# Kernel tuning notes

Hardware: AMD Instinct MI355X
Metric: run time of the kernel (lower is better)

The kernel has to match this reference:

```python
import jax, jax.numpy as jnp
import numpy as np

N = 50000        # nodes
E_RAND = 800000  # random edges (avg degree 16)
F_IN = 512       # num_features
H = 128          # h_dim * num_heads = 16 * 8
C = 40           # num_classes
NEG_SLOPE = 0.2  # GATv2 default


def _glorot(key, shape):
    lim = float(np.sqrt(6.0 / (shape[0] + shape[1])))
    return jax.random.uniform(key, shape, jnp.float32, -lim, lim)


def setup_inputs() -> dict:
    key = jax.random.key(0)
    ks = jax.random.split(key, 12)
    src = jax.random.randint(ks[0], (E_RAND,), 0, N)
    dst = jax.random.randint(ks[1], (E_RAND,), 0, N)
    loop = jnp.arange(N)  # self-loops (GATv2Conv add_self_loops=True)
    edge_index = jnp.stack([jnp.concatenate([src, loop]),
                            jnp.concatenate([dst, loop])]).astype(jnp.int32)
    x = jax.random.normal(ks[2], (N, F_IN), jnp.float32)
    return {
        "x": x,
        "edge_index": edge_index,
        "W1l": _glorot(ks[3], (F_IN, H)), "b1l": jnp.zeros((H,), jnp.float32),
        "W1r": _glorot(ks[4], (F_IN, H)), "b1r": jnp.zeros((H,), jnp.float32),
        "a1": _glorot(ks[5], (H, 1)).reshape(H),
        "bias1": jnp.zeros((H,), jnp.float32),
        "W2l": _glorot(ks[6], (H, C)), "b2l": jnp.zeros((C,), jnp.float32),
        "W2r": _glorot(ks[7], (H, C)), "b2r": jnp.zeros((C,), jnp.float32),
        "a2": _glorot(ks[8], (C, 1)).reshape(C),
        "bias2": jnp.zeros((C,), jnp.float32),
    }


def gatv2_layer(x, src, dst, Wl, bl, Wr, br, att, bias, n):
    # PyG GATv2Conv, heads=1: xl = lin_l(x) (source side), xr = lin_r(x) (target side)
    xl = x @ Wl + bl                                   # [N, C_out]
    xr = x @ Wr + br                                   # [N, C_out]
    # edge score e_ij = a^T LeakyReLU(xl[j] + xr[i])
    e = jax.nn.leaky_relu(xl[src] + xr[dst], negative_slope=NEG_SLOPE) @ att  # [E]
    # segment softmax over edges grouped by destination node
    m = jax.ops.segment_max(e, dst, num_segments=n)    # every node has a self-loop
    ex = jnp.exp(e - m[dst])
    den = jax.ops.segment_sum(ex, dst, num_segments=n)
    alpha = ex / den[dst]                              # [E]
    # weighted scatter-aggregate of source-transformed features
    out = jax.ops.segment_sum(alpha[:, None] * xl[src], dst, num_segments=n)
    return out + bias


def reference(x, edge_index, W1l, b1l, W1r, b1r, a1, bias1,
              W2l, b2l, W2r, b2r, a2, bias2):
    # eval mode: dropout(p=0.6) is identity
    src, dst = edge_index[0], edge_index[1]
    n = x.shape[0]
    h = gatv2_layer(x, src, dst, W1l, b1l, W1r, b1r, a1, bias1, n)
    h = jax.nn.elu(h)
    h = gatv2_layer(h, src, dst, W2l, b2l, W2r, b2r, a2, bias2, n)
    return (h, jax.nn.log_softmax(h, axis=1))
```

## Files before the change

### kernel.cpp

```cpp
#include <hip/hip_runtime.h>
#include <hip/hip_bf16.h>
#include <math.h>

#define FIN 512
#define H1 128
#define C2 40
#define C2P 64

typedef __attribute__((ext_vector_type(8))) short short8;
typedef __attribute__((ext_vector_type(4))) float f32x4;

__device__ __forceinline__ ushort f2bf(float f) {
    union { float f; unsigned u; } c; c.f = f;
    unsigned u = c.u;
    return (ushort)((u + 0x7fffu + ((u >> 16) & 1u)) >> 16);
}
__device__ __forceinline__ float bf2f_lo(unsigned u) { return __uint_as_float(u << 16); }
__device__ __forceinline__ float bf2f_hi(unsigned u) { return __uint_as_float(u & 0xffff0000u); }

__device__ __forceinline__ short bfc(float f) {
    __hip_bfloat16 h = __float2bfloat16(f);
    return *reinterpret_cast<short*>(&h);
}

__device__ __forceinline__ void gload_lds16(const void* g, void* l) {
    __builtin_amdgcn_global_load_lds(
        (const __attribute__((address_space(1))) void*)g,
        (__attribute__((address_space(3))) void*)l, 16, 0, 0);
}

__global__ void count_k(const int* __restrict__ dst, int* __restrict__ cnt, int E) {
    int e = blockIdx.x * 256 + threadIdx.x;
    if (e < E) atomicAdd(&cnt[dst[e] + 1], 1);
}

__global__ __launch_bounds__(1024) void scan_k(int* __restrict__ arr, int ntot) {
    __shared__ int part[1024];
    int t = threadIdx.x;
    int chunk = (((ntot + 1023) / 1024) + 3) & ~3;
    int b = t * chunk;
    int s = 0;
    bool full = (b + chunk <= ntot);
    if (full) {
#pragma unroll 4
        for (int j = 0; j < chunk; j += 4) {
            int4 v = *reinterpret_cast<const int4*>(&arr[b + j]);
            s += v.x + v.y + v.z + v.w;
        }
    } else {
        for (int j = b; j < ntot; j++) s += arr[j];
    }
    part[t] = s;
    __syncthreads();
    for (int off = 1; off < 1024; off <<= 1) {
        int v = (t >= off) ? part[t - off] : 0;
        __syncthreads();
        part[t] += v;
        __syncthreads();
    }
    int run = (t == 0) ? 0 : part[t - 1];
    if (full) {
        for (int j = 0; j < chunk; j += 4) {
            int4 v = *reinterpret_cast<const int4*>(&arr[b + j]);
            int r0 = run + v.x, r1 = r0 + v.y, r2 = r1 + v.z, r3 = r2 + v.w;
            *reinterpret_cast<int4*>(&arr[b + j]) = make_int4(r0, r1, r2, r3);
            run = r3;
        }
    } else {
        for (int j = b; j < ntot; j++) { run += arr[j]; arr[j] = run; }
    }
}

__global__ void fill_k(const int* __restrict__ src, const int* __restrict__ dst,
                       const int* __restrict__ rowptr, int* __restrict__ fillp,
                       int* __restrict__ csr, int E) {
    int e = blockIdx.x * 256 + threadIdx.x;
    if (e < E) {
        int d = dst[e];
        int p = atomicAdd(&fillp[d], 1);
        csr[rowptr[d] + p] = src[e];
    }
}

__global__ void prep_k(const float* __restrict__ W1l, const float* __restrict__ W1r,
                       ushort* __restrict__ Wt2) {
    int idx = blockIdx.x * 256 + threadIdx.x;
    int kc  = idx >> 11;
    int rem = idx & 2047;
    int col = rem >> 3;
    int j   = rem & 7;
    int k   = kc * 8 + j;
    float v = (col < H1) ? W1l[k * H1 + col] : W1r[k * H1 + (col - H1)];
    Wt2[idx] = f2bf(v);
}

__global__ void prep2_k(const float* __restrict__ W2l, const float* __restrict__ W2r,
                        ushort* __restrict__ Ws) {
    int idx = blockIdx.x * 256 + threadIdx.x;
    if (idx >= 80 * H1) return;
    int col = idx >> 7;
    int k   = idx & 127;
    float v = (col < C2) ? W2l[k * C2 + col] : W2r[k * C2 + (col - C2)];
    Ws[idx] = f2bf(v);
}

__global__ __launch_bounds__(256, 3) void gemm1_k(
    const float* __restrict__ x, const ushort* __restrict__ Wt2,
    const float* __restrict__ bl, const float* __restrict__ br,
    ushort* __restrict__ xlb, float* __restrict__ xr, int n)
{
    __shared__ ushort As[64][72];
    __shared__ ushort Bs[8 * 256 * 8];

    const int tid  = threadIdx.x;
    const int w    = tid >> 6;
    const int lane = tid & 63;
    const int l15  = lane & 15;
    const int lhi  = lane >> 4;
    const int r0   = blockIdx.x * 64;

    f32x4 acc[4][4];
#pragma unroll
    for (int m = 0; m < 4; m++)
#pragma unroll
        for (int nn = 0; nn < 4; nn++) acc[m][nn] = (f32x4){0.f, 0.f, 0.f, 0.f};

    const int arow = tid >> 2;
    const int akq  = (tid & 3) * 16;
    const int arow_g = min(r0 + arow, n - 1);
    const float* aptr = x + (size_t)arow_g * FIN + akq;

    const char* bsrc = (const char*)Wt2 + (size_t)w * 8192 + (size_t)lane * 16;
    char*       bdst = (char*)Bs + (size_t)w * 8192 + (size_t)lane * 16;

    for (int kk = 0; kk < FIN; kk += 64) {
        const char* bs = bsrc + (size_t)(kk >> 3) * 4096;
#pragma unroll
        for (int i = 0; i < 8; i++)
            gload_lds16(bs + i * 1024, bdst + i * 1024);

        float4 v0 = *reinterpret_cast<const float4*>(aptr + kk);
        float4 v1 = *reinterpret_cast<const float4*>(aptr + kk + 4);
        float4 v2 = *reinterpret_cast<const float4*>(aptr + kk + 8);
        float4 v3 = *reinterpret_cast<const float4*>(aptr + kk + 12);
        short8 h0, h1;
        h0[0] = bfc(v0.x); h0[1] = bfc(v0.y); h0[2] = bfc(v0.z); h0[3] = bfc(v0.w);
        h0[4] = bfc(v1.x); h0[5] = bfc(v1.y); h0[6] = bfc(v1.z); h0[7] = bfc(v1.w);
        h1[0] = bfc(v2.x); h1[1] = bfc(v2.y); h1[2] = bfc(v2.z); h1[3] = bfc(v2.w);
        h1[4] = bfc(v3.x); h1[5] = bfc(v3.y); h1[6] = bfc(v3.z); h1[7] = bfc(v3.w);
        *reinterpret_cast<short8*>(&As[arow][akq])     = h0;
        *reinterpret_cast<short8*>(&As[arow][akq + 8]) = h1;

        __syncthreads();

#pragma unroll
        for (int ks = 0; ks < 2; ks++) {
            short8 af[4], bf4[4];
#pragma unroll
            for (int m = 0; m < 4; m++)
                af[m] = *reinterpret_cast<const short8*>(&As[m * 16 + l15][ks * 32 + lhi * 8]);
#pragma unroll
            for (int nn = 0; nn < 4; nn++)
                bf4[nn] = *reinterpret_cast<const short8*>(
                    &Bs[((ks * 4 + lhi) * 256 + w * 64 + nn * 16 + l15) * 8]);
#pragma unroll
            for (int m = 0; m < 4; m++)
#pragma unroll
                for (int nn = 0; nn < 4; nn++)
                    acc[m][nn] = __builtin_amdgcn_mfma_f32_16x16x32_bf16(af[m], bf4[nn], acc[m][nn], 0, 0, 0);
        }
        __syncthreads();
    }

#pragma unroll
    for (int nn = 0; nn < 4; nn++) {
        int col = w * 64 + nn * 16 + l15;
        bool left = (col < H1);
        float bias = left ? bl[col] : br[col - H1];
#pragma unroll
        for (int m = 0; m < 4; m++) {
#pragma unroll
            for (int r = 0; r < 4; r++) {
                int row = r0 + m * 16 + lhi * 4 + r;
                if (row < n) {
                    float v = acc[m][nn][r] + bias;
                    if (left) xlb[(size_t)row * H1 + col] = f2bf(v);
                    else      xr [(size_t)row * H1 + (col - H1)] = v;
                }
            }
        }
    }
}

__global__ __launch_bounds__(256) void edge1_k(
    const ushort* __restrict__ xlb, const float* xr,
    const int* __restrict__ rowptr, const int* __restrict__ csr,
    const float* __restrict__ att, const float* __restrict__ bias,
    float* h, int n)
{
    int wid  = threadIdx.x >> 6;
    int lane = threadIdx.x & 63;
    int grp  = lane >> 4;
    int gl   = lane & 15;
    int i = blockIdx.x * 4 + wid;
    if (i >= n) return;

    const float* xrp = &xr[(size_t)i * H1 + gl * 8];
    float4 xr0 = *reinterpret_cast<const float4*>(xrp);
    float4 xr1v = *reinterpret_cast<const float4*>(xrp + 4);
    float xrv[8] = {xr0.x, xr0.y, xr0.z, xr0.w, xr1v.x, xr1v.y, xr1v.z, xr1v.w};
    float4 a0 = *reinterpret_cast<const float4*>(&att[gl * 8]);
    float4 a1 = *reinterpret_cast<const float4*>(&att[gl * 8 + 4]);
    float av[8] = {a0.x, a0.y, a0.z, a0.w, a1.x, a1.y, a1.z, a1.w};

    int e0 = rowptr[i], e1 = rowptr[i + 1];

    float m = -INFINITY, den = 0.f;
    float acc[8];
#pragma unroll
    for (int f = 0; f < 8; f++) acc[f] = 0.f;

    int e = e0 + grp;
    uint4 u;
    if (e < e1) {
        int s = csr[e];
        u = *reinterpret_cast<const uint4*>(&xlb[(size_t)s * H1 + gl * 8]);
    }
    while (e < e1) {
        uint4 cu = u;
        int en = e + 4;
        if (en < e1) {
            int s2 = csr[en];
            u = *reinterpret_cast<const uint4*>(&xlb[(size_t)s2 * H1 + gl * 8]);
        }
        float xlv[8];
        xlv[0] = bf2f_lo(cu.x); xlv[1] = bf2f_hi(cu.x);
        xlv[2] = bf2f_lo(cu.y); xlv[3] = bf2f_hi(cu.y);
        xlv[4] = bf2f_lo(cu.z); xlv[5] = bf2f_hi(cu.z);
        xlv[6] = bf2f_lo(cu.w); xlv[7] = bf2f_hi(cu.w);
        float p = 0.f;
#pragma unroll
        for (int f = 0; f < 8; f++) {
            float t = xlv[f] + xrv[f];
            t = t > 0.f ? t : 0.2f * t;
            p += t * av[f];
        }
#pragma unroll
        for (int o = 8; o > 0; o >>= 1) p += __shfl_xor(p, o);
        float mn = fmaxf(m, p);
        float sc = __expf(m - mn);
        float wgt = __expf(p - mn);
        den = den * sc + wgt;
#pragma unroll
        for (int f = 0; f < 8; f++) acc[f] = acc[f] * sc + wgt * xlv[f];
        m = mn;
        e = en;
    }

    float mstar = m;
    mstar = fmaxf(mstar, __shfl_xor(mstar, 16));
    mstar = fmaxf(mstar, __shfl_xor(mstar, 32));
    float scale = __expf(m - mstar);
    den *= scale;
#pragma unroll
    for (int f = 0; f < 8; f++) acc[f] *= scale;
    den += __shfl_xor(den, 16); den += __shfl_xor(den, 32);
#pragma unroll
    for (int f = 0; f < 8; f++) {
        acc[f] += __shfl_xor(acc[f], 16);
        acc[f] += __shfl_xor(acc[f], 32);
    }

    if (grp == 0) {
        float inv = 1.f / den;
        float o[8];
#pragma unroll
        for (int f = 0; f < 8; f++) {
            float v = acc[f] * inv + bias[gl * 8 + f];
            o[f] = v > 0.f ? v : expm1f(v);
        }
        float* hp = &h[(size_t)i * H1 + gl * 8];
        *reinterpret_cast<float4*>(hp)     = make_float4(o[0], o[1], o[2], o[3]);
        *reinterpret_cast<float4*>(hp + 4) = make_float4(o[4], o[5], o[6], o[7]);
    }
}

__global__ __launch_bounds__(256) void gemm2_k(
    const float* __restrict__ h, const ushort* __restrict__ Ws,
    const float* __restrict__ bl, const float* __restrict__ br,
    ushort* __restrict__ xl2b, float* __restrict__ xr2, int n)
{
    __shared__ ushort WsL[80][136];

    const int tid = threadIdx.x;
    const int w    = tid >> 6;
    const int lane = tid & 63;
    const int l15  = lane & 15;
    const int lhi  = lane >> 4;
    const int r0 = blockIdx.x * 64;

#pragma unroll
    for (int q = 0; q < 5; q++) {
        int c = tid + q * 256;
        int col = c >> 4;
        int k0  = (c & 15) * 8;
        *reinterpret_cast<short8*>(&WsL[col][k0]) =
            *reinterpret_cast<const short8*>(&Ws[col * H1 + k0]);
    }
    __syncthreads();

    const int arow = min(r0 + w * 16 + l15, n - 1);
    const float* ap = &h[(size_t)arow * H1 + lhi * 8];

    f32x4 acc[5];
#pragma unroll
    for (int nt = 0; nt < 5; nt++) acc[nt] = (f32x4){0.f, 0.f, 0.f, 0.f};

#pragma unroll
    for (int kc = 0; kc < 4; kc++) {
        float4 v0 = *reinterpret_cast<const float4*>(ap + kc * 32);
        float4 v1 = *reinterpret_cast<const float4*>(ap + kc * 32 + 4);
        short8 af;
        af[0] = bfc(v0.x); af[1] = bfc(v0.y);
        af[2] = bfc(v0.z); af[3] = bfc(v0.w);
        af[4] = bfc(v1.x); af[5] = bfc(v1.y);
        af[6] = bfc(v1.z); af[7] = bfc(v1.w);
#pragma unroll
        for (int nt = 0; nt < 5; nt++) {
            short8 bf = *reinterpret_cast<const short8*>(&WsL[nt * 16 + l15][kc * 32 + lhi * 8]);
            acc[nt] = __builtin_amdgcn_mfma_f32_16x16x32_bf16(af, bf, acc[nt], 0, 0, 0);
        }
    }

#pragma unroll
    for (int nt = 0; nt < 5; nt++) {
        int col = nt * 16 + l15;
        float bias = (col < C2) ? bl[col] : br[col - C2];
#pragma unroll
        for (int r = 0; r < 4; r++) {
            int row = r0 + w * 16 + lhi * 4 + r;
            if (row < n) {
                float v = acc[nt][r] + bias;
                if (col < C2) xl2b[(size_t)row * C2P + col] = f2bf(v);
                else          xr2 [(size_t)row * C2  + (col - C2)] = v;
            }
        }
    }
    {
        int row = r0 + w * 16 + l15;
        int part = lhi;
        if (part < 3 && row < n) {
            uint4 z = make_uint4(0u, 0u, 0u, 0u);
            *reinterpret_cast<uint4*>(&xl2b[(size_t)row * C2P + C2 + part * 8]) = z;
        }
    }
}

__global__ __launch_bounds__(256) void edge2_k(
    const ushort* __restrict__ xl2b, const float* __restrict__ xr2,
    const int* __restrict__ rowptr, const int* __restrict__ csr,
    const float* __restrict__ att, const float* __restrict__ bias,
    float* __restrict__ out, int n)
{
    int wid  = threadIdx.x >> 6;
    int lane = threadIdx.x & 63;
    int grp  = lane >> 3;
    int gl   = lane & 7;
    int i = blockIdx.x * 4 + wid;
    if (i >= n) return;

    float xrv[8], av[8];
#pragma unroll
    for (int f = 0; f < 8; f++) {
        int idx = gl * 8 + f;
        bool real = idx < C2;
        xrv[f] = real ? xr2[(size_t)i * C2 + idx] : 0.f;
        av[f]  = real ? att[idx] : 0.f;
    }

    int e0 = rowptr[i], e1 = rowptr[i + 1];

    float m = -INFINITY, den = 0.f;
    float acc[8];
#pragma unroll
    for (int f = 0; f < 8; f++) acc[f] = 0.f;

    int e = e0 + grp;
    uint4 u;
    if (e < e1) {
        int s = csr[e];
        u = *reinterpret_cast<const uint4*>(&xl2b[(size_t)s * C2P + gl * 8]);
    }
    while (e < e1) {
        uint4 cu = u;
        int en = e + 8;
        if (en < e1) {
            int s2 = csr[en];
            u = *reinterpret_cast<const uint4*>(&xl2b[(size_t)s2 * C2P + gl * 8]);
        }
        float xlv[8];
        xlv[0] = bf2f_lo(cu.x); xlv[1] = bf2f_hi(cu.x);
        xlv[2] = bf2f_lo(cu.y); xlv[3] = bf2f_hi(cu.y);
        xlv[4] = bf2f_lo(cu.z); xlv[5] = bf2f_hi(cu.z);
        xlv[6] = bf2f_lo(cu.w); xlv[7] = bf2f_hi(cu.w);
        float p = 0.f;
#pragma unroll
        for (int f = 0; f < 8; f++) {
            float t = xlv[f] + xrv[f];
            t = t > 0.f ? t : 0.2f * t;
            p += t * av[f];
        }
#pragma unroll
        for (int o = 4; o > 0; o >>= 1) p += __shfl_xor(p, o);
        float mn = fmaxf(m, p);
        float sc = __expf(m - mn);
        float wgt = __expf(p - mn);
        den = den * sc + wgt;
#pragma unroll
        for (int f = 0; f < 8; f++) acc[f] = acc[f] * sc + wgt * xlv[f];
        m = mn;
        e = en;
    }

    float mstar = m;
    mstar = fmaxf(mstar, __shfl_xor(mstar, 8));
    mstar = fmaxf(mstar, __shfl_xor(mstar, 16));
    mstar = fmaxf(mstar, __shfl_xor(mstar, 32));
    float scale = __expf(m - mstar);
    den *= scale;
#pragma unroll
    for (int f = 0; f < 8; f++) acc[f] *= scale;
    den += __shfl_xor(den, 8); den += __shfl_xor(den, 16); den += __shfl_xor(den, 32);
#pragma unroll
    for (int f = 0; f < 8; f++) {
        acc[f] += __shfl_xor(acc[f], 8);
        acc[f] += __shfl_xor(acc[f], 16);
        acc[f] += __shfl_xor(acc[f], 32);
    }

    float inv = 1.f / den;
    bool real_lane = gl < 5;
    float o[8];
#pragma unroll
    for (int f = 0; f < 8; f++) {
        int idx = gl * 8 + f;
        o[f] = acc[f] * inv + (idx < C2 ? bias[idx] : 0.f);
    }

    float mv = -INFINITY;
    if (real_lane) {
#pragma unroll
        for (int f = 0; f < 8; f++) mv = fmaxf(mv, o[f]);
    }
    mv = fmaxf(mv, __shfl_xor(mv, 1));
    mv = fmaxf(mv, __shfl_xor(mv, 2));
    mv = fmaxf(mv, __shfl_xor(mv, 4));
    float se = 0.f;
    if (real_lane) {
#pragma unroll
        for (int f = 0; f < 8; f++) se += __expf(o[f] - mv);
    }
    se += __shfl_xor(se, 1); se += __shfl_xor(se, 2); se += __shfl_xor(se, 4);
    float lse = mv + logf(se);

    if (grp == 0 && real_lane) {
        float* op = &out[(size_t)i * C2 + gl * 8];
        *reinterpret_cast<float4*>(op)     = make_float4(o[0], o[1], o[2], o[3]);
        *reinterpret_cast<float4*>(op + 4) = make_float4(o[4], o[5], o[6], o[7]);
        float* lp = &out[(size_t)n * C2 + (size_t)i * C2 + gl * 8];
        *reinterpret_cast<float4*>(lp)     = make_float4(o[0] - lse, o[1] - lse, o[2] - lse, o[3] - lse);
        *reinterpret_cast<float4*>(lp + 4) = make_float4(o[4] - lse, o[5] - lse, o[6] - lse, o[7] - lse);
    }
}

extern "C" void kernel_launch(void* const* d_in, const int* in_sizes, int n_in,
                              void* d_out, int out_size, void* d_ws, size_t ws_size,
                              hipStream_t stream) {
    const float* x    = (const float*)d_in[0];
    const int*   ei   = (const int*)  d_in[1];
    const float* W1l  = (const float*)d_in[2];
    const float* b1l  = (const float*)d_in[3];
    const float* W1r  = (const float*)d_in[4];
    const float* b1r  = (const float*)d_in[5];
    const float* a1   = (const float*)d_in[6];
    const float* bias1= (const float*)d_in[7];
    const float* W2l  = (const float*)d_in[8];
    const float* b2l  = (const float*)d_in[9];
    const float* W2r  = (const float*)d_in[10];
    const float* b2r  = (const float*)d_in[11];
    const float* a2   = (const float*)d_in[12];
    const float* bias2= (const float*)d_in[13];

    const int N = in_sizes[0] / FIN;
    const int E = in_sizes[1] / 2;
    const int* src = ei;
    const int* dst = ei + E;

    float*  xr1 = (float*)d_ws;
    float*  xr2 = xr1 + (size_t)N * H1;
    ushort* xlb = (ushort*)(xr2 + (size_t)N * C2);
    ushort* xl2b = xlb;
    ushort* Wt2 = xlb + (size_t)N * H1;
    ushort* Ws2 = Wt2 + 131072;
    int* rowptr = (int*)(Ws2 + 10240);
    int* fillp  = rowptr + (N + 1);
    int* csr    = fillp + N;

    hipMemsetAsync(rowptr, 0, sizeof(int) * (size_t)(2 * N + 1), stream);
    count_k<<<(E + 255) / 256, 256, 0, stream>>>(dst, rowptr, E);
    scan_k<<<1, 1024, 0, stream>>>(rowptr, N + 1);
    fill_k<<<(E + 255) / 256, 256, 0, stream>>>(src, dst, rowptr, fillp, csr, E);

    prep_k<<<512, 256, 0, stream>>>(W1l, W1r, Wt2);
    prep2_k<<<40, 256, 0, stream>>>(W2l, W2r, Ws2);
    gemm1_k<<<(N + 63) / 64, 256, 0, stream>>>(x, Wt2, b1l, b1r, xlb, xr1, N);
    edge1_k<<<(N + 3) / 4, 256, 0, stream>>>(xlb, xr1, rowptr, csr, a1, bias1, xr1, N);
    gemm2_k<<<(N + 63) / 64, 256, 0, stream>>>(xr1, Ws2, b2l, b2r, xl2b, xr2, N);
    edge2_k<<<(N + 3) / 4, 256, 0, stream>>>(xl2b, xr2, rowptr, csr, a2, bias2, (float*)d_out, N);
}
```

Baseline: 294.6 us.

## Double-buffer GEMM1 LDS tiles and deepen gather prefetch in aggregation kernels

The first-layer GEMM moves from single-buffered 64-wide K tiles to double-buffered 32-wide K tiles. The next tile's global-to-LDS loads and x conversion are issued before the MFMAs on the current tile, and one barrier per step replaces two. Both edge-aggregation kernels now prefetch the gathered source features two iterations ahead instead of one, to hide more gather latency. The cost is more register pressure from the extra uint4 buffer, and the GEMM runs twice as many, smaller iterations.

```diff
diff --git a/kernel.cpp b/kernel.cpp
--- a/kernel.cpp
+++ b/kernel.cpp
@@ -109,8 +109,8 @@
     const float* __restrict__ bl, const float* __restrict__ br,
     ushort* __restrict__ xlb, float* __restrict__ xr, int n)
 {
-    __shared__ ushort As[64][72];
-    __shared__ ushort Bs[8 * 256 * 8];
+    __shared__ ushort As[2][64][40];
+    __shared__ ushort Bs[2][4 * 256 * 8];
 
     const int tid  = threadIdx.x;
     const int w    = tid >> 6;
@@ -126,50 +126,77 @@
         for (int nn = 0; nn < 4; nn++) acc[m][nn] = (f32x4){0.f, 0.f, 0.f, 0.f};
 
     const int arow = tid >> 2;
-    const int akq  = (tid & 3) * 16;
+    const int akq  = (tid & 3) * 8;
     const int arow_g = min(r0 + arow, n - 1);
     const float* aptr = x + (size_t)arow_g * FIN + akq;
 
-    const char* bsrc = (const char*)Wt2 + (size_t)w * 8192 + (size_t)lane * 16;
-    char*       bdst = (char*)Bs + (size_t)w * 8192 + (size_t)lane * 16;
-
-    for (int kk = 0; kk < FIN; kk += 64) {
-        const char* bs = bsrc + (size_t)(kk >> 3) * 4096;
-#pragma unroll
-        for (int i = 0; i < 8; i++)
-            gload_lds16(bs + i * 1024, bdst + i * 1024);
-
-        float4 v0 = *reinterpret_cast<const float4*>(aptr + kk);
-        float4 v1 = *reinterpret_cast<const float4*>(aptr + kk + 4);
-        float4 v2 = *reinterpret_cast<const float4*>(aptr + kk + 8);
-        float4 v3 = *reinterpret_cast<const float4*>(aptr + kk + 12);
-        short8 h0, h1;
+    const char* bsrc = (const char*)Wt2 + (size_t)tid * 16;
+    char*       bdst = (char*)Bs + (size_t)tid * 16;
+
+    {
+        float4 v0 = *reinterpret_cast<const float4*>(aptr);
+        float4 v1 = *reinterpret_cast<const float4*>(aptr + 4);
+#pragma unroll
+        for (int i = 0; i < 4; i++)
+            gload_lds16(bsrc + i * 4096, bdst + i * 4096);
+        short8 h0;
         h0[0] = bfc(v0.x); h0[1] = bfc(v0.y); h0[2] = bfc(v0.z); h0[3] = bfc(v0.w);
         h0[4] = bfc(v1.x); h0[5] = bfc(v1.y); h0[6] = bfc(v1.z); h0[7] = bfc(v1.w);
-        h1[0] = bfc(v2.x); h1[1] = bfc(v2.y); h1[2] = bfc(v2.z); h1[3] = bfc(v2.w);
-        h1[4] = bfc(v3.x); h1[5] = bfc(v3.y); h1[6] = bfc(v3.z); h1[7] = bfc(v3.w);
-        *reinterpret_cast<short8*>(&As[arow][akq])     = h0;
-        *reinterpret_cast<short8*>(&As[arow][akq + 8]) = h1;
+        *reinterpret_cast<short8*>(&As[0][arow][akq]) = h0;
+    }
+    __syncthreads();
+
+    int cur = 0;
+    for (int t = 0; t < 15; ++t) {
+        const int nxt = cur ^ 1;
+
+        float4 v0 = *reinterpret_cast<const float4*>(aptr + (t + 1) * 32);
+        float4 v1 = *reinterpret_cast<const float4*>(aptr + (t + 1) * 32 + 4);
+        {
+            const char* bs = bsrc + (size_t)(t + 1) * 16384;
+            char*       bd = bdst + (size_t)nxt * 16384;
+#pragma unroll
+            for (int i = 0; i < 4; i++)
+                gload_lds16(bs + i * 4096, bd + i * 4096);
+        }
+
+        short8 af[4], bf4[4];
+#pragma unroll
+        for (int m = 0; m < 4; m++)
+            af[m] = *reinterpret_cast<const short8*>(&As[cur][m * 16 + l15][lhi * 8]);
+#pragma unroll
+        for (int nn = 0; nn < 4; nn++)
+            bf4[nn] = *reinterpret_cast<const short8*>(
+                &Bs[cur][(lhi * 256 + w * 64 + nn * 16 + l15) * 8]);
+#pragma unroll
+        for (int m = 0; m < 4; m++)
+#pragma unroll
+            for (int nn = 0; nn < 4; nn++)
+                acc[m][nn] = __builtin_amdgcn_mfma_f32_16x16x32_bf16(af[m], bf4[nn], acc[m][nn], 0, 0, 0);
+
+        short8 h0;
+        h0[0] = bfc(v0.x); h0[1] = bfc(v0.y); h0[2] = bfc(v0.z); h0[3] = bfc(v0.w);
+        h0[4] = bfc(v1.x); h0[5] = bfc(v1.y); h0[6] = bfc(v1.z); h0[7] = bfc(v1.w);
+        *reinterpret_cast<short8*>(&As[nxt][arow][akq]) = h0;
 
         __syncthreads();
-
-#pragma unroll
-        for (int ks = 0; ks < 2; ks++) {
-            short8 af[4], bf4[4];
-#pragma unroll
-            for (int m = 0; m < 4; m++)
-                af[m] = *reinterpret_cast<const short8*>(&As[m * 16 + l15][ks * 32 + lhi * 8]);
+        cur = nxt;
+    }
+
+    {
+        short8 af[4], bf4[4];
+#pragma unroll
+        for (int m = 0; m < 4; m++)
+            af[m] = *reinterpret_cast<const short8*>(&As[cur][m * 16 + l15][lhi * 8]);
+#pragma unroll
+        for (int nn = 0; nn < 4; nn++)
+            bf4[nn] = *reinterpret_cast<const short8*>(
+                &Bs[cur][(lhi * 256 + w * 64 + nn * 16 + l15) * 8]);
+#pragma unroll
+        for (int m = 0; m < 4; m++)
 #pragma unroll
             for (int nn = 0; nn < 4; nn++)
-                bf4[nn] = *reinterpret_cast<const short8*>(
-                    &Bs[((ks * 4 + lhi) * 256 + w * 64 + nn * 16 + l15) * 8]);
-#pragma unroll
-            for (int m = 0; m < 4; m++)
-#pragma unroll
-                for (int nn = 0; nn < 4; nn++)
-                    acc[m][nn] = __builtin_amdgcn_mfma_f32_16x16x32_bf16(af[m], bf4[nn], acc[m][nn], 0, 0, 0);
-        }
-        __syncthreads();
+                acc[m][nn] = __builtin_amdgcn_mfma_f32_16x16x32_bf16(af[m], bf4[nn], acc[m][nn], 0, 0, 0);
     }
 
 #pragma unroll
@@ -221,17 +248,21 @@
     for (int f = 0; f < 8; f++) acc[f] = 0.f;
 
     int e = e0 + grp;
-    uint4 u;
+    uint4 u0, u1;
     if (e < e1) {
         int s = csr[e];
-        u = *reinterpret_cast<const uint4*>(&xlb[(size_t)s * H1 + gl * 8]);
+        u0 = *reinterpret_cast<const uint4*>(&xlb[(size_t)s * H1 + gl * 8]);
+    }
+    if (e + 4 < e1) {
+        int s = csr[e + 4];
+        u1 = *reinterpret_cast<const uint4*>(&xlb[(size_t)s * H1 + gl * 8]);
     }
     while (e < e1) {
-        uint4 cu = u;
-        int en = e + 4;
-        if (en < e1) {
-            int s2 = csr[en];
-            u = *reinterpret_cast<const uint4*>(&xlb[(size_t)s2 * H1 + gl * 8]);
+        uint4 cu = u0;
+        u0 = u1;
+        if (e + 8 < e1) {
+            int s2 = csr[e + 8];
+            u1 = *reinterpret_cast<const uint4*>(&xlb[(size_t)s2 * H1 + gl * 8]);
         }
         float xlv[8];
         xlv[0] = bf2f_lo(cu.x); xlv[1] = bf2f_hi(cu.x);
@@ -254,7 +285,7 @@
 #pragma unroll
         for (int f = 0; f < 8; f++) acc[f] = acc[f] * sc + wgt * xlv[f];
         m = mn;
-        e = en;
+        e += 4;
     }
 
     float mstar = m;
@@ -386,17 +417,21 @@
     for (int f = 0; f < 8; f++) acc[f] = 0.f;
 
     int e = e0 + grp;
-    uint4 u;
+    uint4 u0, u1;
     if (e < e1) {
         int s = csr[e];
-        u = *reinterpret_cast<const uint4*>(&xl2b[(size_t)s * C2P + gl * 8]);
+        u0 = *reinterpret_cast<const uint4*>(&xl2b[(size_t)s * C2P + gl * 8]);
+    }
+    if (e + 8 < e1) {
+        int s = csr[e + 8];
+        u1 = *reinterpret_cast<const uint4*>(&xl2b[(size_t)s * C2P + gl * 8]);
     }
     while (e < e1) {
-        uint4 cu = u;
-        int en = e + 8;
-        if (en < e1) {
-            int s2 = csr[en];
-            u = *reinterpret_cast<const uint4*>(&xl2b[(size_t)s2 * C2P + gl * 8]);
+        uint4 cu = u0;
+        u0 = u1;
+        if (e + 16 < e1) {
+            int s2 = csr[e + 16];
+            u1 = *reinterpret_cast<const uint4*>(&xl2b[(size_t)s2 * C2P + gl * 8]);
         }
         float xlv[8];
         xlv[0] = bf2f_lo(cu.x); xlv[1] = bf2f_hi(cu.x);
@@ -419,7 +454,7 @@
 #pragma unroll
         for (int f = 0; f < 8; f++) acc[f] = acc[f] * sc + wgt * xlv[f];
         m = mn;
-        e = en;
+        e += 8;
     }
 
     float mstar = m;
```

Result: slower. 306.3 us (+4.0%).

## Fuse layer-2 linear into edge1 aggregation and merge prep kernels into count

Applied to the files above, without the earlier changes.

Merges the count, weight-prep and layer-2 weight-prep kernels into one launch, and fuses the second GEMM into the first edge kernel. Each wave now computes its node's h row, stages it in LDS and does the 128x80 dot products with scalar FMAs, so the fp32 h tensor is never written to or read back from global memory. Edge1 switches to 8 lanes per edge with 16 features each and a two-deep gather prefetch, and edge2 gets the same deeper prefetch. The cost is more register pressure, per-block weight loading into LDS in edge1, and scalar FMAs in place of MFMA for the small GEMM. xl2b gets its own workspace buffer instead of aliasing xlb.

```diff
diff --git a/kernel.cpp b/kernel.cpp
--- a/kernel.cpp
+++ b/kernel.cpp
@@ -17,6 +17,9 @@
 }
 __device__ __forceinline__ float bf2f_lo(unsigned u) { return __uint_as_float(u << 16); }
 __device__ __forceinline__ float bf2f_hi(unsigned u) { return __uint_as_float(u & 0xffff0000u); }
+__device__ __forceinline__ float bf2f_s(short s) {
+    return __uint_as_float(((unsigned)(ushort)s) << 16);
+}
 
 __device__ __forceinline__ short bfc(float f) {
     __hip_bfloat16 h = __float2bfloat16(f);
@@ -29,9 +32,34 @@
         (__attribute__((address_space(3))) void*)l, 16, 0, 0);
 }
 
-__global__ void count_k(const int* __restrict__ dst, int* __restrict__ cnt, int E) {
-    int e = blockIdx.x * 256 + threadIdx.x;
-    if (e < E) atomicAdd(&cnt[dst[e] + 1], 1);
+__global__ void aux_k(const int* __restrict__ dst, int* __restrict__ cnt, int E, int EB,
+                      const float* __restrict__ W1l, const float* __restrict__ W1r,
+                      ushort* __restrict__ Wt2,
+                      const float* __restrict__ W2l, const float* __restrict__ W2r,
+                      ushort* __restrict__ Ws) {
+    int b = blockIdx.x;
+    int t = threadIdx.x;
+    if (b < EB) {
+        int e = b * 256 + t;
+        if (e < E) atomicAdd(&cnt[dst[e] + 1], 1);
+    } else if (b < EB + 512) {
+        int idx = (b - EB) * 256 + t;
+        int kc  = idx >> 11;
+        int rem = idx & 2047;
+        int col = rem >> 3;
+        int j   = rem & 7;
+        int k   = kc * 8 + j;
+        float v = (col < H1) ? W1l[k * H1 + col] : W1r[k * H1 + (col - H1)];
+        Wt2[idx] = f2bf(v);
+    } else {
+        int idx = (b - EB - 512) * 256 + t;
+        if (idx < 80 * H1) {
+            int col = idx >> 7;
+            int k   = idx & 127;
+            float v = (col < C2) ? W2l[k * C2 + col] : W2r[k * C2 + (col - C2)];
+            Ws[idx] = f2bf(v);
+        }
+    }
 }
 
 __global__ __launch_bounds__(1024) void scan_k(int* __restrict__ arr, int ntot) {
@@ -82,28 +110,6 @@
     }
 }
 
-__global__ void prep_k(const float* __restrict__ W1l, const float* __restrict__ W1r,
-                       ushort* __restrict__ Wt2) {
-    int idx = blockIdx.x * 256 + threadIdx.x;
-    int kc  = idx >> 11;
-    int rem = idx & 2047;
-    int col = rem >> 3;
-    int j   = rem & 7;
-    int k   = kc * 8 + j;
-    float v = (col < H1) ? W1l[k * H1 + col] : W1r[k * H1 + (col - H1)];
-    Wt2[idx] = f2bf(v);
-}
-
-__global__ void prep2_k(const float* __restrict__ W2l, const float* __restrict__ W2r,
-                        ushort* __restrict__ Ws) {
-    int idx = blockIdx.x * 256 + threadIdx.x;
-    if (idx >= 80 * H1) return;
-    int col = idx >> 7;
-    int k   = idx & 127;
-    float v = (col < C2) ? W2l[k * C2 + col] : W2r[k * C2 + (col - C2)];
-    Ws[idx] = f2bf(v);
-}
-
 __global__ __launch_bounds__(256, 3) void gemm1_k(
     const float* __restrict__ x, const ushort* __restrict__ Wt2,
     const float* __restrict__ bl, const float* __restrict__ br,
@@ -193,112 +199,17 @@
 }
 
 __global__ __launch_bounds__(256) void edge1_k(
-    const ushort* __restrict__ xlb, const float* xr,
+    const ushort* __restrict__ xlb, const float* __restrict__ xr,
     const int* __restrict__ rowptr, const int* __restrict__ csr,
     const float* __restrict__ att, const float* __restrict__ bias,
-    float* h, int n)
-{
-    int wid  = threadIdx.x >> 6;
-    int lane = threadIdx.x & 63;
-    int grp  = lane >> 4;
-    int gl   = lane & 15;
-    int i = blockIdx.x * 4 + wid;
-    if (i >= n) return;
-
-    const float* xrp = &xr[(size_t)i * H1 + gl * 8];
-    float4 xr0 = *reinterpret_cast<const float4*>(xrp);
-    float4 xr1v = *reinterpret_cast<const float4*>(xrp + 4);
-    float xrv[8] = {xr0.x, xr0.y, xr0.z, xr0.w, xr1v.x, xr1v.y, xr1v.z, xr1v.w};
-    float4 a0 = *reinterpret_cast<const float4*>(&att[gl * 8]);
-    float4 a1 = *reinterpret_cast<const float4*>(&att[gl * 8 + 4]);
-    float av[8] = {a0.x, a0.y, a0.z, a0.w, a1.x, a1.y, a1.z, a1.w};
-
-    int e0 = rowptr[i], e1 = rowptr[i + 1];
-
-    float m = -INFINITY, den = 0.f;
-    float acc[8];
-#pragma unroll
-    for (int f = 0; f < 8; f++) acc[f] = 0.f;
-
-    int e = e0 + grp;
-    uint4 u;
-    if (e < e1) {
-        int s = csr[e];
-        u = *reinterpret_cast<const uint4*>(&xlb[(size_t)s * H1 + gl * 8]);
-    }
-    while (e < e1) {
-        uint4 cu = u;
-        int en = e + 4;
-        if (en < e1) {
-            int s2 = csr[en];
-            u = *reinterpret_cast<const uint4*>(&xlb[(size_t)s2 * H1 + gl * 8]);
-        }
-        float xlv[8];
-        xlv[0] = bf2f_lo(cu.x); xlv[1] = bf2f_hi(cu.x);
-        xlv[2] = bf2f_lo(cu.y); xlv[3] = bf2f_hi(cu.y);
-        xlv[4] = bf2f_lo(cu.z); xlv[5] = bf2f_hi(cu.z);
-        xlv[6] = bf2f_lo(cu.w); xlv[7] = bf2f_hi(cu.w);
-        float p = 0.f;
-#pragma unroll
-        for (int f = 0; f < 8; f++) {
-            float t = xlv[f] + xrv[f];
-            t = t > 0.f ? t : 0.2f * t;
-            p += t * av[f];
-        }
-#pragma unroll
-        for (int o = 8; o > 0; o >>= 1) p += __shfl_xor(p, o);
-        float mn = fmaxf(m, p);
-        float sc = __expf(m - mn);
-        float wgt = __expf(p - mn);
-        den = den * sc + wgt;
-#pragma unroll
-        for (int f = 0; f < 8; f++) acc[f] = acc[f] * sc + wgt * xlv[f];
-        m = mn;
-        e = en;
-    }
-
-    float mstar = m;
-    mstar = fmaxf(mstar, __shfl_xor(mstar, 16));
-    mstar = fmaxf(mstar, __shfl_xor(mstar, 32));
-    float scale = __expf(m - mstar);
-    den *= scale;
-#pragma unroll
-    for (int f = 0; f < 8; f++) acc[f] *= scale;
-    den += __shfl_xor(den, 16); den += __shfl_xor(den, 32);
-#pragma unroll
-    for (int f = 0; f < 8; f++) {
-        acc[f] += __shfl_xor(acc[f], 16);
-        acc[f] += __shfl_xor(acc[f], 32);
-    }
-
-    if (grp == 0) {
-        float inv = 1.f / den;
-        float o[8];
-#pragma unroll
-        for (int f = 0; f < 8; f++) {
-            float v = acc[f] * inv + bias[gl * 8 + f];
-            o[f] = v > 0.f ? v : expm1f(v);
-        }
-        float* hp = &h[(size_t)i * H1 + gl * 8];
-        *reinterpret_cast<float4*>(hp)     = make_float4(o[0], o[1], o[2], o[3]);
-        *reinterpret_cast<float4*>(hp + 4) = make_float4(o[4], o[5], o[6], o[7]);
-    }
-}
-
-__global__ __launch_bounds__(256) void gemm2_k(
-    const float* __restrict__ h, const ushort* __restrict__ Ws,
-    const float* __restrict__ bl, const float* __restrict__ br,
+    const ushort* __restrict__ Ws, const float* __restrict__ b2l,
+    const float* __restrict__ b2r,
     ushort* __restrict__ xl2b, float* __restrict__ xr2, int n)
 {
     __shared__ ushort WsL[80][136];
+    __shared__ float  hlds[4][128];
 
     const int tid = threadIdx.x;
-    const int w    = tid >> 6;
-    const int lane = tid & 63;
-    const int l15  = lane & 15;
-    const int lhi  = lane >> 4;
-    const int r0 = blockIdx.x * 64;
-
 #pragma unroll
     for (int q = 0; q < 5; q++) {
         int c = tid + q * 256;
@@ -309,50 +220,136 @@
     }
     __syncthreads();
 
-    const int arow = min(r0 + w * 16 + l15, n - 1);
-    const float* ap = &h[(size_t)arow * H1 + lhi * 8];
-
-    f32x4 acc[5];
-#pragma unroll
-    for (int nt = 0; nt < 5; nt++) acc[nt] = (f32x4){0.f, 0.f, 0.f, 0.f};
-
-#pragma unroll
-    for (int kc = 0; kc < 4; kc++) {
-        float4 v0 = *reinterpret_cast<const float4*>(ap + kc * 32);
-        float4 v1 = *reinterpret_cast<const float4*>(ap + kc * 32 + 4);
-        short8 af;
-        af[0] = bfc(v0.x); af[1] = bfc(v0.y);
-        af[2] = bfc(v0.z); af[3] = bfc(v0.w);
-        af[4] = bfc(v1.x); af[5] = bfc(v1.y);
-        af[6] = bfc(v1.z); af[7] = bfc(v1.w);
-#pragma unroll
-        for (int nt = 0; nt < 5; nt++) {
-            short8 bf = *reinterpret_cast<const short8*>(&WsL[nt * 16 + l15][kc * 32 + lhi * 8]);
-            acc[nt] = __builtin_amdgcn_mfma_f32_16x16x32_bf16(af, bf, acc[nt], 0, 0, 0);
-        }
-    }
-
-#pragma unroll
-    for (int nt = 0; nt < 5; nt++) {
-        int col = nt * 16 + l15;
-        float bias = (col < C2) ? bl[col] : br[col - C2];
-#pragma unroll
-        for (int r = 0; r < 4; r++) {
-            int row = r0 + w * 16 + lhi * 4 + r;
-            if (row < n) {
-                float v = acc[nt][r] + bias;
-                if (col < C2) xl2b[(size_t)row * C2P + col] = f2bf(v);
-                else          xr2 [(size_t)row * C2  + (col - C2)] = v;
+    const int wid  = tid >> 6;
+    const int lane = tid & 63;
+    const int grp  = lane >> 3;
+    const int gl   = lane & 7;
+    const int i = blockIdx.x * 4 + wid;
+    if (i >= n) return;
+
+    float xrv[16], av[16];
+    {
+        const float* p  = &xr[(size_t)i * H1 + gl * 16];
+        const float* pa = &att[gl * 16];
+#pragma unroll
+        for (int q = 0; q < 4; q++) {
+            float4 v = *reinterpret_cast<const float4*>(p + q * 4);
+            xrv[q*4+0]=v.x; xrv[q*4+1]=v.y; xrv[q*4+2]=v.z; xrv[q*4+3]=v.w;
+            float4 a = *reinterpret_cast<const float4*>(pa + q * 4);
+            av[q*4+0]=a.x; av[q*4+1]=a.y; av[q*4+2]=a.z; av[q*4+3]=a.w;
+        }
+    }
+
+    int e0 = rowptr[i], e1 = rowptr[i + 1];
+
+    float m = -INFINITY, den = 0.f;
+    float acc[16];
+#pragma unroll
+    for (int f = 0; f < 16; f++) acc[f] = 0.f;
+
+    int e = e0 + grp;
+    uint4 ua0, ub0, ua1, ub1;
+    if (e < e1) {
+        const ushort* p = &xlb[(size_t)csr[e] * H1 + gl * 16];
+        ua0 = *reinterpret_cast<const uint4*>(p);
+        ub0 = *reinterpret_cast<const uint4*>(p + 8);
+    }
+    if (e + 8 < e1) {
+        const ushort* p = &xlb[(size_t)csr[e + 8] * H1 + gl * 16];
+        ua1 = *reinterpret_cast<const uint4*>(p);
+        ub1 = *reinterpret_cast<const uint4*>(p + 8);
+    }
+    while (e < e1) {
+        uint4 ca = ua0, cb = ub0;
+        ua0 = ua1; ub0 = ub1;
+        if (e + 16 < e1) {
+            const ushort* p = &xlb[(size_t)csr[e + 16] * H1 + gl * 16];
+            ua1 = *reinterpret_cast<const uint4*>(p);
+            ub1 = *reinterpret_cast<const uint4*>(p + 8);
+        }
+        float xlv[16];
+        xlv[0]  = bf2f_lo(ca.x); xlv[1]  = bf2f_hi(ca.x);
+        xlv[2]  = bf2f_lo(ca.y); xlv[3]  = bf2f_hi(ca.y);
+        xlv[4]  = bf2f_lo(ca.z); xlv[5]  = bf2f_hi(ca.z);
+        xlv[6]  = bf2f_lo(ca.w); xlv[7]  = bf2f_hi(ca.w);
+        xlv[8]  = bf2f_lo(cb.x); xlv[9]  = bf2f_hi(cb.x);
+        xlv[10] = bf2f_lo(cb.y); xlv[11] = bf2f_hi(cb.y);
+        xlv[12] = bf2f_lo(cb.z); xlv[13] = bf2f_hi(cb.z);
+        xlv[14] = bf2f_lo(cb.w); xlv[15] = bf2f_hi(cb.w);
+        float p = 0.f;
+#pragma unroll
+        for (int f = 0; f < 16; f++) {
+            float t = xlv[f] + xrv[f];
+            t = t > 0.f ? t : 0.2f * t;
+            p += t * av[f];
+        }
+        p += __shfl_xor(p, 4); p += __shfl_xor(p, 2); p += __shfl_xor(p, 1);
+        float mn = fmaxf(m, p);
+        float sc = __expf(m - mn);
+        float wgt = __expf(p - mn);
+        den = den * sc + wgt;
+#pragma unroll
+        for (int f = 0; f < 16; f++) acc[f] = acc[f] * sc + wgt * xlv[f];
+        m = mn;
+        e += 8;
+    }
+
+    float mstar = m;
+    mstar = fmaxf(mstar, __shfl_xor(mstar, 8));
+    mstar = fmaxf(mstar, __shfl_xor(mstar, 16));
+    mstar = fmaxf(mstar, __shfl_xor(mstar, 32));
+    float scale = __expf(m - mstar);
+    den *= scale;
+#pragma unroll
+    for (int f = 0; f < 16; f++) acc[f] *= scale;
+    den += __shfl_xor(den, 8); den += __shfl_xor(den, 16); den += __shfl_xor(den, 32);
+#pragma unroll
+    for (int f = 0; f < 16; f++) {
+        acc[f] += __shfl_xor(acc[f], 8);
+        acc[f] += __shfl_xor(acc[f], 16);
+        acc[f] += __shfl_xor(acc[f], 32);
+    }
+
+    float inv = 1.f / den;
+    float o[16];
+#pragma unroll
+    for (int f = 0; f < 16; f++) {
+        float v = acc[f] * inv + bias[gl * 16 + f];
+        o[f] = v > 0.f ? v : expm1f(v);
+    }
+
+    if (grp == 0) {
+#pragma unroll
+        for (int q = 0; q < 4; q++)
+            *reinterpret_cast<float4*>(&hlds[wid][gl * 16 + q * 4]) =
+                make_float4(o[q*4], o[q*4+1], o[q*4+2], o[q*4+3]);
+    }
+
+#pragma unroll
+    for (int pass = 0; pass < 2; pass++) {
+        int c = (pass == 0) ? lane : 64 + lane;
+        bool active = (pass == 0) || (lane < 16);
+        if (active) {
+            float s2 = 0.f;
+#pragma unroll
+            for (int kb = 0; kb < 16; kb++) {
+                float4 hA = *reinterpret_cast<const float4*>(&hlds[wid][kb * 8]);
+                float4 hB = *reinterpret_cast<const float4*>(&hlds[wid][kb * 8 + 4]);
+                short8 wv = *reinterpret_cast<const short8*>(&WsL[c][kb * 8]);
+                s2 = fmaf(hA.x, bf2f_s(wv[0]), s2);
+                s2 = fmaf(hA.y, bf2f_s(wv[1]), s2);
+                s2 = fmaf(hA.z, bf2f_s(wv[2]), s2);
+                s2 = fmaf(hA.w, bf2f_s(wv[3]), s2);
+                s2 = fmaf(hB.x, bf2f_s(wv[4]), s2);
+                s2 = fmaf(hB.y, bf2f_s(wv[5]), s2);
+                s2 = fmaf(hB.z, bf2f_s(wv[6]), s2);
+                s2 = fmaf(hB.w, bf2f_s(wv[7]), s2);
             }
-        }
-    }
-    {
-        int row = r0 + w * 16 + l15;
-        int part = lhi;
-        if (part < 3 && row < n) {
-            uint4 z = make_uint4(0u, 0u, 0u, 0u);
-            *reinterpret_cast<uint4*>(&xl2b[(size_t)row * C2P + C2 + part * 8]) = z;
-        }
+            if (c < C2) xl2b[(size_t)i * C2P + c] = f2bf(s2 + b2l[c]);
+            else        xr2 [(size_t)i * C2 + (c - C2)] = s2 + b2r[c - C2];
+        }
+        if (pass == 0 && lane >= C2)
+            xl2b[(size_t)i * C2P + lane] = 0;
     }
 }
 
@@ -386,17 +383,21 @@
     for (int f = 0; f < 8; f++) acc[f] = 0.f;
 
     int e = e0 + grp;
-    uint4 u;
+    uint4 u0, u1;
     if (e < e1) {
         int s = csr[e];
-        u = *reinterpret_cast<const uint4*>(&xl2b[(size_t)s * C2P + gl * 8]);
+        u0 = *reinterpret_cast<const uint4*>(&xl2b[(size_t)s * C2P + gl * 8]);
+    }
+    if (e + 8 < e1) {
+        int s = csr[e + 8];
+        u1 = *reinterpret_cast<const uint4*>(&xl2b[(size_t)s * C2P + gl * 8]);
     }
     while (e < e1) {
-        uint4 cu = u;
-        int en = e + 8;
-        if (en < e1) {
-            int s2 = csr[en];
-            u = *reinterpret_cast<const uint4*>(&xl2b[(size_t)s2 * C2P + gl * 8]);
+        uint4 cu = u0;
+        u0 = u1;
+        if (e + 16 < e1) {
+            int s2 = csr[e + 16];
+            u1 = *reinterpret_cast<const uint4*>(&xl2b[(size_t)s2 * C2P + gl * 8]);
         }
         float xlv[8];
         xlv[0] = bf2f_lo(cu.x); xlv[1] = bf2f_hi(cu.x);
@@ -419,7 +420,7 @@
 #pragma unroll
         for (int f = 0; f < 8; f++) acc[f] = acc[f] * sc + wgt * xlv[f];
         m = mn;
-        e = en;
+        e += 8;
     }
 
     float mstar = m;
@@ -496,25 +497,25 @@
     const int* src = ei;
     const int* dst = ei + E;
 
-    float*  xr1 = (float*)d_ws;
-    float*  xr2 = xr1 + (size_t)N * H1;
-    ushort* xlb = (ushort*)(xr2 + (size_t)N * C2);
-    ushort* xl2b = xlb;
-    ushort* Wt2 = xlb + (size_t)N * H1;
-    ushort* Ws2 = Wt2 + 131072;
-    int* rowptr = (int*)(Ws2 + 10240);
-    int* fillp  = rowptr + (N + 1);
-    int* csr    = fillp + N;
+    float*  xr1  = (float*)d_ws;
+    float*  xr2  = xr1 + (size_t)N * H1;
+    ushort* xlb  = (ushort*)(xr2 + (size_t)N * C2);
+    ushort* xl2b = xlb + (size_t)N * H1;
+    ushort* Wt2  = xl2b + (size_t)N * C2P;
+    ushort* Ws2  = Wt2 + 131072;
+    int* rowptr  = (int*)(Ws2 + 10240);
+    int* fillp   = rowptr + (N + 1);
+    int* csr     = fillp + N;
+
+    const int EB = (E + 255) / 256;
 
     hipMemsetAsync(rowptr, 0, sizeof(int) * (size_t)(2 * N + 1), stream);
-    count_k<<<(E + 255) / 256, 256, 0, stream>>>(dst, rowptr, E);
+    aux_k<<<EB + 552, 256, 0, stream>>>(dst, rowptr, E, EB, W1l, W1r, Wt2, W2l, W2r, Ws2);
     scan_k<<<1, 1024, 0, stream>>>(rowptr, N + 1);
-    fill_k<<<(E + 255) / 256, 256, 0, stream>>>(src, dst, rowptr, fillp, csr, E);
-
-    prep_k<<<512, 256, 0, stream>>>(W1l, W1r, Wt2);
-    prep2_k<<<40, 256, 0, stream>>>(W2l, W2r, Ws2);
+    fill_k<<<EB, 256, 0, stream>>>(src, dst, rowptr, fillp, csr, E);
+
     gemm1_k<<<(N + 63) / 64, 256, 0, stream>>>(x, Wt2, b1l, b1r, xlb, xr1, N);
-    edge1_k<<<(N + 3) / 4, 256, 0, stream>>>(xlb, xr1, rowptr, csr, a1, bias1, xr1, N);
-    gemm2_k<<<(N + 63) / 64, 256, 0, stream>>>(xr1, Ws2, b2l, b2r, xl2b, xr2, N);
+    edge1_k<<<(N + 3) / 4, 256, 0, stream>>>(xlb, xr1, rowptr, csr, a1, bias1,
+                                             Ws2, b2l, b2r, xl2b, xr2, N);
     edge2_k<<<(N + 3) / 4, 256, 0, stream>>>(xl2b, xr2, rowptr, csr, a2, bias2, (float*)d_out, N);
 }
```

Result: slower. 397.9 us (+35.1%).
